# Optimization experiments

Measured on AMD Instinct MI355X. Metric: run time of the kernel, lower is better.

## Reference

```python
import jax, jax.numpy as jnp
import numpy as np

K, STRIDE, PAD, DIL = 3, 1, 1, 1


def setup_inputs() -> dict:
    key = jax.random.key(0)
    k0, k1, k2, k3, k4 = jax.random.split(key, 5)
    B, Cin, Cout, H, W = 16, 64, 64, 64, 64
    x = jax.random.normal(k0, (B, Cin, H, W), dtype=jnp.float32)
    # NOTE: the torch module zero-inits conv_offset; we use small random
    # weights so the deformable sampling path is actually exercised.
    w_off = jax.random.normal(k1, (2 * K * K, Cin, K, K), dtype=jnp.float32) * 0.01
    b_off = jax.random.normal(k2, (2 * K * K,), dtype=jnp.float32) * 0.01
    fan_in = Cin * K * K
    w_dcn = jax.random.normal(k3, (Cout, Cin, K, K), dtype=jnp.float32) / np.sqrt(fan_in)
    b_dcn = jax.random.normal(k4, (Cout,), dtype=jnp.float32) * 0.01
    return {"x": x, "w_off": w_off, "b_off": b_off, "w_dcn": w_dcn, "b_dcn": b_dcn}


def _conv2d(x, w, b, stride, pad):
    out = jax.lax.conv_general_dilated(
        x, w, window_strides=(stride, stride), padding=[(pad, pad), (pad, pad)],
        dimension_numbers=("NCHW", "OIHW", "NCHW"))
    return out + b[None, :, None, None]


def _deform_conv(x, offset, w, b, stride, pad, dil):
    # torchvision-style DeformConv2d, groups=1, no modulation mask.
    B, Cin, H, W = x.shape
    Cout = w.shape[0]
    Ho = (H + 2 * pad - dil * (K - 1) - 1) // stride + 1
    Wo = (W + 2 * pad - dil * (K - 1) - 1) // stride + 1
    KK = K * K
    # base sampling grid: p0 + dilation*kernel_tap + learned offset
    oy = (jnp.arange(Ho) * stride - pad).astype(x.dtype)
    ox = (jnp.arange(Wo) * stride - pad).astype(x.dtype)
    ky, kx = jnp.meshgrid(jnp.arange(K), jnp.arange(K), indexing="ij")
    ky = (ky * dil).reshape(-1).astype(x.dtype)  # [KK], row (y) of tap
    kx = (kx * dil).reshape(-1).astype(x.dtype)
    # offset channel layout: [y_0, x_0, y_1, x_1, ...] -> [B, KK, 2, Ho, Wo]
    off = offset.reshape(B, KK, 2, Ho, Wo)
    py = off[:, :, 0] + ky[None, :, None, None] + oy[None, None, :, None]  # [B,KK,Ho,Wo]
    px = off[:, :, 1] + kx[None, :, None, None] + ox[None, None, None, :]
    y0 = jnp.floor(py)
    x0 = jnp.floor(px)
    wy1 = py - y0
    wx1 = px - x0
    wy0 = 1.0 - wy1
    wx0 = 1.0 - wx1
    x_flat = x.reshape(B, Cin, H * W)

    def gather(yi, xi):
        valid = (yi >= 0) & (yi < H) & (xi >= 0) & (xi < W)  # zero padding outside
        yc = jnp.clip(yi, 0, H - 1).astype(jnp.int32)
        xc = jnp.clip(xi, 0, W - 1).astype(jnp.int32)
        idx = (yc * W + xc).reshape(B, 1, -1)
        v = jnp.take_along_axis(x_flat, idx, axis=2).reshape(B, Cin, KK, Ho, Wo)
        return v * valid.astype(x.dtype).reshape(B, 1, KK, Ho, Wo)

    cols = (gather(y0, x0) * (wy0 * wx0)[:, None]
            + gather(y0, x0 + 1) * (wy0 * wx1)[:, None]
            + gather(y0 + 1, x0) * (wy1 * wx0)[:, None]
            + gather(y0 + 1, x0 + 1) * (wy1 * wx1)[:, None])  # [B,Cin,KK,Ho,Wo]
    out = jnp.einsum("bckhw,ock->bohw", cols, w.reshape(Cout, Cin, KK))
    return out + b[None, :, None, None]


def reference(x, w_off, b_off, w_dcn, b_dcn):
    offset = _conv2d(x, w_off, b_off, STRIDE, PAD)
    return _deform_conv(x, offset, w_dcn, b_dcn, STRIDE, PAD, DIL)
```

## Files before the change

### kernel.cpp

```cpp
#include <hip/hip_runtime.h>
#include <hip/hip_fp16.h>


#define KOFF 18
#define CPAD 72
#define GSTR 33

#define W2T_HALFS    (18 * 64 * 32)
#define WOFF2T_HALFS (18 * 32 * 32)
#define W2T_BYTES    (W2T_HALFS * 2)
#define WOFF2T_OFF   W2T_BYTES
#define X_OFF        (W2T_BYTES + WOFF2T_HALFS * 2)
#define XH_BYTES     (16 * 64 * 64 * 64 * 2)
#define WS_NEED      (X_OFF + XH_BYTES)

typedef _Float16 half8 __attribute__((ext_vector_type(8)));
typedef float floatx4 __attribute__((ext_vector_type(4)));

union H8 { half8 v; __half2 h2[4]; uint4 u; };

__global__ void prep(const float* __restrict__ x,
                     const float* __restrict__ w_dcn,
                     const float* __restrict__ w_off,
                     _Float16* __restrict__ w2t,
                     _Float16* __restrict__ woff2t,
                     _Float16* __restrict__ xh) {
    const int bi = blockIdx.x;
    const int t  = threadIdx.x;
    if (bi < 1024) {
        const int b = bi >> 6, y = bi & 63;
        __shared__ __align__(16) _Float16 tile[64 * CPAD];
        const int xx = t & 63;
        const int c4 = t >> 6;
        const float* xp = x + (((size_t)b * 64) * 64 + y) * 64;
#pragma unroll
        for (int p = 0; p < 16; ++p) {
            int cin = p * 4 + c4;
            tile[xx * CPAD + cin] = (_Float16)xp[(size_t)cin * 4096 + xx];
        }
        __syncthreads();
        const int oct = t & 7;
        const int xl  = t >> 3;
        _Float16* op = xh + ((((size_t)b * 64 + y) * 64) << 6);
#pragma unroll
        for (int p = 0; p < 2; ++p) {
            int xr = p * 32 + xl;
            half8 v = *(const half8*)&tile[xr * CPAD + oct * 8];
            *(half8*)&op[(size_t)xr * 64 + oct * 8] = v;
        }
    } else {
        int e = (bi - 1024) * 256 + t;
        if (e < W2T_HALFS) {
            int kl = e & 31, co = (e >> 5) & 63, i = e >> 11;
            int tap = i >> 1, cin = (i & 1) * 32 + kl;
            w2t[e] = (_Float16)w_dcn[co * 576 + cin * 9 + tap];
        } else {
            int e2 = e - W2T_HALFS;
            int kl = e2 & 31, co = (e2 >> 5) & 31, i = e2 >> 10;
            int tap = i >> 1, cin = (i & 1) * 32 + kl;
            woff2t[e2] = (co < KOFF) ? (_Float16)w_off[co * 576 + cin * 9 + tap]
                                     : (_Float16)0.f;
        }
    }
}

__launch_bounds__(256, 4)
__global__ void dcn_main(const _Float16* __restrict__ xh,
                         const _Float16* __restrict__ w2t,
                         const _Float16* __restrict__ woff2t,
                         const float* __restrict__ b_off,
                         const float* __restrict__ b_dcn,
                         float* __restrict__ out) {
    const int bid = blockIdx.x;
    const int s   = bid >> 3;
    const int b   = ((bid & 7) << 1) | (s >> 7);
    const int ho  = (s >> 1) & 63;
    const int hlf = s & 1;
    const int t    = threadIdx.x;
    const int lane = t & 63;
    const int wid  = __builtin_amdgcn_readfirstlane(t >> 6);
    const int r    = lane & 15;
    const int q    = lane >> 4;
    const int gpx  = t >> 3;
    const int oct  = t & 7;
    const int pxg  = hlf * 32;

    __shared__ __align__(16) _Float16 colsT[2][32 * CPAD];
    __shared__ __align__(16) float    offlds[KOFF * 32];
    __shared__ __align__(16) uint4    grecL[9 * GSTR];

    const _Float16* xb = xh + ((size_t)b << 18);
    const char* xpb = (const char*)xb;

    {
        floatx4 am = {0.f, 0.f, 0.f, 0.f};
        const int m = wid & 1, n = wid >> 1;

        auto loadS = [&](int tap) -> half8 {
            const int dy = tap / 3, dxk = tap - dy * 3;
            const int y  = ho + dy - 1;
            const int xc = pxg + gpx + dxk - 1;
            half8 v = {};
            if (((unsigned)y < 64u) && ((unsigned)xc < 64u))
                v = *(const half8*)&xb[(((size_t)y * 64 + xc) << 6) + oct * 8];
            return v;
        };
        auto loadWA = [&](int tap, int g) -> half8 {
            return *(const half8*)&woff2t[(tap * 2 + g) * 1024
                                          + (m * 16 + r) * 32 + q * 8];
        };

        half8 sv = loadS(0);
        *(half8*)&colsT[0][gpx * CPAD + oct * 8] = sv;
        half8 a0 = loadWA(0, 0), a1 = loadWA(0, 1);
        __syncthreads();
#pragma unroll
        for (int tap = 0; tap < 9; ++tap) {
            half8 sn, a0n, a1n;
            if (tap < 8) {
                sn  = loadS(tap + 1);
                a0n = loadWA(tap + 1, 0);
                a1n = loadWA(tap + 1, 1);
            }
            half8 bf0 = *(const half8*)&colsT[tap & 1][(n * 16 + r) * CPAD + q * 8];
            half8 bf1 = *(const half8*)&colsT[tap & 1][(n * 16 + r) * CPAD + 32 + q * 8];
            am = __builtin_amdgcn_mfma_f32_16x16x32_f16(a0, bf0, am, 0, 0, 0);
            am = __builtin_amdgcn_mfma_f32_16x16x32_f16(a1, bf1, am, 0, 0, 0);
            if (tap < 8) {
                *(half8*)&colsT[(tap + 1) & 1][gpx * CPAD + oct * 8] = sn;
                a0 = a0n; a1 = a1n;
            }
            __syncthreads();
        }
#pragma unroll
        for (int reg = 0; reg < 4; ++reg) {
            int co = m * 16 + q * 4 + reg;
            if (co < KOFF)
                offlds[co * 32 + n * 16 + r] = am[reg] + b_off[co];
        }
    }
    __syncthreads();

    for (int e = t; e < 9 * 32; e += 256) {
        int tap = e >> 5, px = e & 31;
        float offy = offlds[(2 * tap) * 32 + px];
        float offx = offlds[(2 * tap + 1) * 32 + px];
        float py  = offy + (float)(tap / 3) + (float)(ho - 1);
        float pxf = offx + (float)(tap % 3) + (float)(pxg + px - 1);
        float fy = floorf(py), fx = floorf(pxf);
        int y0 = (int)fy, x0 = (int)fx;
        float wy1 = py - fy, wx1 = pxf - fx;
        float wy0 = 1.f - wy1, wx0 = 1.f - wx1;
        bool y0ok = ((unsigned)y0 < 64u);
        bool x0ok = ((unsigned)x0 < 64u);
        bool y1ok = ((unsigned)(y0 + 1) < 64u);
        bool x1ok = ((unsigned)(x0 + 1) < 64u);
        float w00 = (y0ok && x0ok) ? wy0 * wx0 : 0.f;
        float w01 = (y0ok && x1ok) ? wy0 * wx1 : 0.f;
        float w10 = (y1ok && x0ok) ? wy1 * wx0 : 0.f;
        float w11 = (y1ok && x1ok) ? wy1 * wx1 : 0.f;
        int yc0 = min(max(y0, 0), 63);
        int xc0 = min(max(x0, 0), 63);
        int yc1 = min(max(y0 + 1, 0), 63);
        int xc1 = min(max(x0 + 1, 0), 63);
        union { __half2 h; unsigned u; } c0, c1;
        c0.h = __floats2half2_rn(w00, w01);
        c1.h = __floats2half2_rn(w10, w11);
        uint4 rec;
        rec.x = (unsigned)(yc0 * 64 + xc0)
              | ((unsigned)(xc1 - xc0) << 12)
              | ((unsigned)(yc1 - yc0) << 13);
        rec.y = c0.u;
        rec.z = c1.u;
        rec.w = 0u;
        grecL[tap * GSTR + px] = rec;
    }
    __syncthreads();

    floatx4 acc0 = {0.f, 0.f, 0.f, 0.f};
    floatx4 acc1 = {0.f, 0.f, 0.f, 0.f};

    struct G { H8 a, c, d, e; unsigned wy, wz; };

    auto loadB = [&](int tap) -> G {
        uint4 rec = grecL[tap * GSTR + gpx];
        unsigned a00 = (rec.x & 0xfffu) * 128u + (unsigned)oct * 16u;
        unsigned dx128  = ((rec.x >> 12) & 1u) * 128u;
        unsigned dy8192 = ((rec.x >> 13) & 1u) * 8192u;
        G g;
        g.a.v = *(const half8*)(xpb + a00);
        g.c.v = *(const half8*)(xpb + a00 + dx128);
        g.d.v = *(const half8*)(xpb + a00 + dy8192);
        g.e.v = *(const half8*)(xpb + a00 + dy8192 + dx128);
        g.wy = rec.y; g.wz = rec.z;
        return g;
    };
    auto storeB = [&](int tap, G& g) {
        union { unsigned u; __half2 h; } cy, cz;
        cy.u = g.wy; cz.u = g.wz;
        __half2 W00 = __half2half2(__low2half(cy.h));
        __half2 W01 = __half2half2(__high2half(cy.h));
        __half2 W10 = __half2half2(__low2half(cz.h));
        __half2 W11 = __half2half2(__high2half(cz.h));
        H8 res;
#pragma unroll
        for (int c = 0; c < 4; ++c) {
            __half2 aa = __hmul2(g.a.h2[c], W00);
            aa = __hfma2(g.c.h2[c], W01, aa);
            aa = __hfma2(g.d.h2[c], W10, aa);
            aa = __hfma2(g.e.h2[c], W11, aa);
            res.h2[c] = aa;
        }
        *(half8*)&colsT[tap & 1][gpx * CPAD + oct * 8] = res.v;
    };
    auto loadW = [&](int tap, int g) -> half8 {
        return *(const half8*)&w2t[(size_t)(tap * 2 + g) * 2048
                                   + (wid * 16 + r) * 32 + q * 8];
    };

    {
        G g0 = loadB(0);
        storeB(0, g0);
    }
    half8 af0 = loadW(0, 0), af1 = loadW(0, 1);
    __syncthreads();
#pragma unroll
    for (int tap = 0; tap < 9; ++tap) {
        G gn;
        half8 af0n, af1n;
        if (tap < 8) {
            gn   = loadB(tap + 1);
            af0n = loadW(tap + 1, 0);
            af1n = loadW(tap + 1, 1);
        }
        half8 b00 = *(const half8*)&colsT[tap & 1][r * CPAD + q * 8];
        half8 b10 = *(const half8*)&colsT[tap & 1][(16 + r) * CPAD + q * 8];
        half8 b01 = *(const half8*)&colsT[tap & 1][r * CPAD + 32 + q * 8];
        half8 b11 = *(const half8*)&colsT[tap & 1][(16 + r) * CPAD + 32 + q * 8];
        acc0 = __builtin_amdgcn_mfma_f32_16x16x32_f16(af0, b00, acc0, 0, 0, 0);
        acc1 = __builtin_amdgcn_mfma_f32_16x16x32_f16(af0, b10, acc1, 0, 0, 0);
        acc0 = __builtin_amdgcn_mfma_f32_16x16x32_f16(af1, b01, acc0, 0, 0, 0);
        acc1 = __builtin_amdgcn_mfma_f32_16x16x32_f16(af1, b11, acc1, 0, 0, 0);
        if (tap < 8) {
            storeB(tap + 1, gn);
            af0 = af0n; af1 = af1n;
            __syncthreads();
        }
    }

#pragma unroll
    for (int reg = 0; reg < 4; ++reg) {
        int co = wid * 16 + q * 4 + reg;
        float bias = b_dcn[co];
        size_t o = (((size_t)b * 64 + co) * 64 + ho) * 64 + pxg;
        out[o + r]      = acc0[reg] + bias;
        out[o + 16 + r] = acc1[reg] + bias;
    }
}

#define FCPAD 40
__launch_bounds__(256, 4)
__global__ void dcn_fb(const float* __restrict__ x,
                       const float* __restrict__ w_dcn,
                       const float* __restrict__ w_off,
                       const float* __restrict__ b_off,
                       const float* __restrict__ b_dcn,
                       float* __restrict__ out) {
    const int bid = blockIdx.x;
    const int s   = bid >> 3;
    const int b   = ((bid & 7) << 1) | (s >> 7);
    const int ho  = (s >> 1) & 63;
    const int hlf = s & 1;
    const int t    = threadIdx.x;
    const int lane = t & 63;
    const int wid  = __builtin_amdgcn_readfirstlane(t >> 6);
    const int r    = lane & 15;
    const int q    = lane >> 4;
    const int px   = t & 31;
    const int kq   = t >> 5;

    __shared__ __align__(16) _Float16 colsT[2][32 * FCPAD];
    __shared__ __align__(16) float    offlds[KOFF * 32];

    const float* xb = x + (size_t)b * 64 * 4096;
    const int pxg = hlf * 32;

    {
        floatx4 am = {0.f, 0.f, 0.f, 0.f};
        const int m = wid & 1, n = wid >> 1;
        auto stageA = [&](int i) {
            const int tap = i >> 1;
            const int dy = tap / 3, dxk = tap - dy * 3;
            const int y  = ho + dy - 1;
            const int xc = pxg + px + dxk - 1;
            const bool ok = ((unsigned)y < 64u) && ((unsigned)xc < 64u);
            const float* xp = xb + ((size_t)((i & 1) * 32 + kq * 4)) * 4096
                                 + y * 64 + xc;
            float va[4];
#pragma unroll
            for (int j = 0; j < 4; ++j) va[j] = ok ? xp[(size_t)j * 4096] : 0.f;
#pragma unroll
            for (int j = 0; j < 4; ++j)
                colsT[i & 1][px * FCPAD + kq * 4 + j] = (_Float16)va[j];
        };
        auto loadA = [&](int i) -> half8 {
            const int tap = i >> 1;
            const int cin0 = (i & 1) * 32 + q * 8;
            const int co = m * 16 + r;
            half8 v;
#pragma unroll
            for (int j = 0; j < 8; ++j)
                v[j] = (co < KOFF) ? (_Float16)w_off[co * 576 + (cin0 + j) * 9 + tap]
                                   : (_Float16)0.f;
            return v;
        };
        stageA(0);
        __syncthreads();
#pragma unroll
        for (int i = 0; i < 18; ++i) {
            if (i < 17) stageA(i + 1);
            half8 a = loadA(i);
            half8 bfr = *(const half8*)&colsT[i & 1][(n * 16 + r) * FCPAD + q * 8];
            am = __builtin_amdgcn_mfma_f32_16x16x32_f16(a, bfr, am, 0, 0, 0);
            __syncthreads();
        }
#pragma unroll
        for (int reg = 0; reg < 4; ++reg) {
            int co = m * 16 + q * 4 + reg;
            if (co < KOFF)
                offlds[co * 32 + (n * 16 + r)] = am[reg] + b_off[co];
        }
    }
    __syncthreads();

    unsigned rmeta[9], rw0[9], rw1[9];
#pragma unroll
    for (int tap = 0; tap < 9; ++tap) {
        float offy = offlds[(2 * tap) * 32 + px];
        float offx = offlds[(2 * tap + 1) * 32 + px];
        float py  = offy + (float)(tap / 3) + (float)(ho - 1);
        float pxf = offx + (float)(tap % 3) + (float)(pxg + px - 1);
        float fy = floorf(py), fx = floorf(pxf);
        int y0 = (int)fy, x0 = (int)fx;
        float wy1 = py - fy, wx1 = pxf - fx;
        float wy0 = 1.f - wy1, wx0 = 1.f - wx1;
        bool y0ok = ((unsigned)y0 < 64u);
        bool x0ok = ((unsigned)x0 < 64u);
        bool y1ok = ((unsigned)(y0 + 1) < 64u);
        bool x1ok = ((unsigned)(x0 + 1) < 64u);
        float w00 = (y0ok && x0ok) ? wy0 * wx0 : 0.f;
        float w01 = (y0ok && x1ok) ? wy0 * wx1 : 0.f;
        float w10 = (y1ok && x0ok) ? wy1 * wx0 : 0.f;
        float w11 = (y1ok && x1ok) ? wy1 * wx1 : 0.f;
        int yc0 = min(max(y0, 0), 63);
        int xc0 = min(max(x0, 0), 63);
        int yc1 = min(max(y0 + 1, 0), 63);
        int xc1 = min(max(x0 + 1, 0), 63);
        union { __half2 h; unsigned u; } c0, c1;
        c0.h = __floats2half2_rn(w00, w01);
        c1.h = __floats2half2_rn(w10, w11);
        rmeta[tap] = (unsigned)(yc0 * 64 + xc0)
                   | ((unsigned)(xc1 - xc0) << 12)
                   | ((unsigned)(yc1 - yc0) << 13);
        rw0[tap] = c0.u;
        rw1[tap] = c1.u;
    }

    floatx4 acc0 = {0.f, 0.f, 0.f, 0.f};
    floatx4 acc1 = {0.f, 0.f, 0.f, 0.f};

    auto gather = [&](int i) {
        const int tap = i >> 1;
        const unsigned m = rmeta[tap];
        const unsigned a00 = (m & 0xfffu) << 2;
        const unsigned a01 = a00 + ((m >> 10) & 4u);
        const unsigned a10 = a00 + ((m >> 5) & 256u);
        const unsigned a11 = a10 + ((m >> 10) & 4u);
        const char* base = (const char*)xb
                         + ((size_t)((i & 1) * 32 + kq * 4)) * 16384;
        float v00[4], v01[4], v10[4], v11[4];
#pragma unroll
        for (int j = 0; j < 4; ++j) {
            const char* xp = base + (size_t)j * 16384;
            v00[j] = *(const float*)(xp + a00);
            v01[j] = *(const float*)(xp + a01);
            v10[j] = *(const float*)(xp + a10);
            v11[j] = *(const float*)(xp + a11);
        }
        union { unsigned u; __half2 h; } c0, c1;
        c0.u = rw0[tap]; c1.u = rw1[tap];
        const float wA = __half2float(c0.h.x), wB = __half2float(c0.h.y);
        const float wC = __half2float(c1.h.x), wD = __half2float(c1.h.y);
#pragma unroll
        for (int j = 0; j < 4; ++j)
            colsT[i & 1][px * FCPAD + kq * 4 + j] =
                (_Float16)(v00[j] * wA + v01[j] * wB + v10[j] * wC + v11[j] * wD);
    };

    auto load_af = [&](int i) -> half8 {
        const int tap = i >> 1;
        const int cin0 = (i & 1) * 32 + q * 8;
        half8 v;
#pragma unroll
        for (int j = 0; j < 8; ++j)
            v[j] = (_Float16)w_dcn[(wid * 16 + r) * 576 + (cin0 + j) * 9 + tap];
        return v;
    };

    gather(0);
    __syncthreads();
#pragma unroll
    for (int i = 0; i < 18; ++i) {
        if (i < 17) gather(i + 1);
        half8 af = load_af(i);
        half8 b0 = *(const half8*)&colsT[i & 1][r * FCPAD + q * 8];
        half8 b1 = *(const half8*)&colsT[i & 1][(16 + r) * FCPAD + q * 8];
        acc0 = __builtin_amdgcn_mfma_f32_16x16x32_f16(af, b0, acc0, 0, 0, 0);
        acc1 = __builtin_amdgcn_mfma_f32_16x16x32_f16(af, b1, acc1, 0, 0, 0);
        if (i < 17) __syncthreads();
    }

#pragma unroll
    for (int reg = 0; reg < 4; ++reg) {
        int co = wid * 16 + q * 4 + reg;
        float bias = b_dcn[co];
        size_t o = (((size_t)b * 64 + co) * 64 + ho) * 64 + pxg;
        out[o + r]      = acc0[reg] + bias;
        out[o + 16 + r] = acc1[reg] + bias;
    }
}

extern "C" void kernel_launch(void* const* d_in, const int* in_sizes, int n_in,
                              void* d_out, int out_size, void* d_ws, size_t ws_size,
                              hipStream_t stream) {
    const float* x     = (const float*)d_in[0];
    const float* w_off = (const float*)d_in[1];
    const float* b_off = (const float*)d_in[2];
    const float* w_dcn = (const float*)d_in[3];
    const float* b_dcn = (const float*)d_in[4];
    float* out = (float*)d_out;

    char* ws = (char*)d_ws;
    _Float16* w2t    = (_Float16*)ws;
    _Float16* woff2t = (_Float16*)(ws + WOFF2T_OFF);
    _Float16* xh     = (_Float16*)(ws + X_OFF);

    if (ws_size >= (size_t)WS_NEED) {
        prep<<<1240, 256, 0, stream>>>(x, w_dcn, w_off, w2t, woff2t, xh);
        dcn_main<<<2048, 256, 0, stream>>>(xh, w2t, woff2t, b_off, b_dcn, out);
    } else {
        dcn_fb<<<2048, 256, 0, stream>>>(x, w_dcn, w_off, b_off, b_dcn, out);
    }
}
```

Baseline: 110.2 us.

## Process two taps per pipeline stage to halve barriers in offset and deform GEMMs

Both the offset-conv and deformable-conv MFMA loops now stage two kernel taps per double-buffered LDS slot, with the column tile widened to 128 halfs plus padding. This cuts the number of __syncthreads from nine to five per phase and gives more independent gathers and MFMAs between barriers, so load latency can be hidden better. In exchange it doubles the bilinear gather registers in flight and grows LDS usage, which may lower occupancy.

```diff
diff --git a/kernel.cpp b/kernel.cpp
--- a/kernel.cpp
+++ b/kernel.cpp
@@ -3,7 +3,7 @@
 
 
 #define KOFF 18
-#define CPAD 72
+#define CTS  136
 #define GSTR 33
 
 #define W2T_HALFS    (18 * 64 * 32)
@@ -29,14 +29,14 @@
     const int t  = threadIdx.x;
     if (bi < 1024) {
         const int b = bi >> 6, y = bi & 63;
-        __shared__ __align__(16) _Float16 tile[64 * CPAD];
+        __shared__ __align__(16) _Float16 tile[64 * 72];
         const int xx = t & 63;
         const int c4 = t >> 6;
         const float* xp = x + (((size_t)b * 64) * 64 + y) * 64;
 #pragma unroll
         for (int p = 0; p < 16; ++p) {
             int cin = p * 4 + c4;
-            tile[xx * CPAD + cin] = (_Float16)xp[(size_t)cin * 4096 + xx];
+            tile[xx * 72 + cin] = (_Float16)xp[(size_t)cin * 4096 + xx];
         }
         __syncthreads();
         const int oct = t & 7;
@@ -45,7 +45,7 @@
 #pragma unroll
         for (int p = 0; p < 2; ++p) {
             int xr = p * 32 + xl;
-            half8 v = *(const half8*)&tile[xr * CPAD + oct * 8];
+            half8 v = *(const half8*)&tile[xr * 72 + oct * 8];
             *(half8*)&op[(size_t)xr * 64 + oct * 8] = v;
         }
     } else {
@@ -85,7 +85,7 @@
     const int oct  = t & 7;
     const int pxg  = hlf * 32;
 
-    __shared__ __align__(16) _Float16 colsT[2][32 * CPAD];
+    __shared__ __align__(16) _Float16 colsT[2][32 * CTS];
     __shared__ __align__(16) float    offlds[KOFF * 32];
     __shared__ __align__(16) uint4    grecL[9 * GSTR];
 
@@ -105,32 +105,39 @@
                 v = *(const half8*)&xb[(((size_t)y * 64 + xc) << 6) + oct * 8];
             return v;
         };
-        auto loadWA = [&](int tap, int g) -> half8 {
-            return *(const half8*)&woff2t[(tap * 2 + g) * 1024
-                                          + (m * 16 + r) * 32 + q * 8];
+        auto loadWA = [&](int i) -> half8 {
+            return *(const half8*)&woff2t[i * 1024 + (m * 16 + r) * 32 + q * 8];
         };
 
-        half8 sv = loadS(0);
-        *(half8*)&colsT[0][gpx * CPAD + oct * 8] = sv;
-        half8 a0 = loadWA(0, 0), a1 = loadWA(0, 1);
+        {
+            half8 s0 = loadS(0), s1 = loadS(1);
+            *(half8*)&colsT[0][gpx * CTS + oct * 8]      = s0;
+            *(half8*)&colsT[0][gpx * CTS + 64 + oct * 8] = s1;
+        }
         __syncthreads();
 #pragma unroll
-        for (int tap = 0; tap < 9; ++tap) {
-            half8 sn, a0n, a1n;
-            if (tap < 8) {
-                sn  = loadS(tap + 1);
-                a0n = loadWA(tap + 1, 0);
-                a1n = loadWA(tap + 1, 1);
-            }
-            half8 bf0 = *(const half8*)&colsT[tap & 1][(n * 16 + r) * CPAD + q * 8];
-            half8 bf1 = *(const half8*)&colsT[tap & 1][(n * 16 + r) * CPAD + 32 + q * 8];
-            am = __builtin_amdgcn_mfma_f32_16x16x32_f16(a0, bf0, am, 0, 0, 0);
-            am = __builtin_amdgcn_mfma_f32_16x16x32_f16(a1, bf1, am, 0, 0, 0);
-            if (tap < 8) {
-                *(half8*)&colsT[(tap + 1) & 1][gpx * CPAD + oct * 8] = sn;
-                a0 = a0n; a1 = a1n;
-            }
-            __syncthreads();
+        for (int p = 0; p < 5; ++p) {
+            half8 sn0, sn1;
+            if (p < 4) {
+                sn0 = loadS(2 * p + 2);
+                if (p < 3) sn1 = loadS(2 * p + 3);
+            }
+            const int nkg = (p < 4) ? 4 : 2;
+#pragma unroll
+            for (int kg = 0; kg < 4; ++kg) {
+                if (kg < nkg) {
+                    half8 a  = loadWA(4 * p + kg);
+                    half8 bf = *(const half8*)&colsT[p & 1][(n * 16 + r) * CTS
+                                                            + kg * 32 + q * 8];
+                    am = __builtin_amdgcn_mfma_f32_16x16x32_f16(a, bf, am, 0, 0, 0);
+                }
+            }
+            if (p < 4) {
+                *(half8*)&colsT[(p + 1) & 1][gpx * CTS + oct * 8] = sn0;
+                if (p < 3)
+                    *(half8*)&colsT[(p + 1) & 1][gpx * CTS + 64 + oct * 8] = sn1;
+                __syncthreads();
+            }
         }
 #pragma unroll
         for (int reg = 0; reg < 4; ++reg) {
@@ -180,70 +187,90 @@
     floatx4 acc0 = {0.f, 0.f, 0.f, 0.f};
     floatx4 acc1 = {0.f, 0.f, 0.f, 0.f};
 
-    struct G { H8 a, c, d, e; unsigned wy, wz; };
-
-    auto loadB = [&](int tap) -> G {
-        uint4 rec = grecL[tap * GSTR + gpx];
-        unsigned a00 = (rec.x & 0xfffu) * 128u + (unsigned)oct * 16u;
-        unsigned dx128  = ((rec.x >> 12) & 1u) * 128u;
-        unsigned dy8192 = ((rec.x >> 13) & 1u) * 8192u;
-        G g;
-        g.a.v = *(const half8*)(xpb + a00);
-        g.c.v = *(const half8*)(xpb + a00 + dx128);
-        g.d.v = *(const half8*)(xpb + a00 + dy8192);
-        g.e.v = *(const half8*)(xpb + a00 + dy8192 + dx128);
-        g.wy = rec.y; g.wz = rec.z;
+    struct GP { H8 v[8]; unsigned wy0, wz0, wy1, wz1; };
+
+    auto loadPairB = [&](int p) -> GP {
+        GP g;
+#pragma unroll
+        for (int l = 0; l < 2; ++l) {
+            int tap = 2 * p + l;
+            if (tap < 9) {
+                uint4 rec = grecL[tap * GSTR + gpx];
+                unsigned a00 = (rec.x & 0xfffu) * 128u + (unsigned)oct * 16u;
+                unsigned dx128  = ((rec.x >> 12) & 1u) * 128u;
+                unsigned dy8192 = ((rec.x >> 13) & 1u) * 8192u;
+                g.v[4 * l + 0].v = *(const half8*)(xpb + a00);
+                g.v[4 * l + 1].v = *(const half8*)(xpb + a00 + dx128);
+                g.v[4 * l + 2].v = *(const half8*)(xpb + a00 + dy8192);
+                g.v[4 * l + 3].v = *(const half8*)(xpb + a00 + dy8192 + dx128);
+                if (l == 0) { g.wy0 = rec.y; g.wz0 = rec.z; }
+                else        { g.wy1 = rec.y; g.wz1 = rec.z; }
+            }
+        }
         return g;
     };
-    auto storeB = [&](int tap, G& g) {
-        union { unsigned u; __half2 h; } cy, cz;
-        cy.u = g.wy; cz.u = g.wz;
-        __half2 W00 = __half2half2(__low2half(cy.h));
-        __half2 W01 = __half2half2(__high2half(cy.h));
-        __half2 W10 = __half2half2(__low2half(cz.h));
-        __half2 W11 = __half2half2(__high2half(cz.h));
-        H8 res;
-#pragma unroll
-        for (int c = 0; c < 4; ++c) {
-            __half2 aa = __hmul2(g.a.h2[c], W00);
-            aa = __hfma2(g.c.h2[c], W01, aa);
-            aa = __hfma2(g.d.h2[c], W10, aa);
-            aa = __hfma2(g.e.h2[c], W11, aa);
-            res.h2[c] = aa;
-        }
-        *(half8*)&colsT[tap & 1][gpx * CPAD + oct * 8] = res.v;
+    auto storePairB = [&](int p, int buf, GP& g) {
+#pragma unroll
+        for (int l = 0; l < 2; ++l) {
+            int tap = 2 * p + l;
+            if (tap < 9) {
+                union { unsigned u; __half2 h; } cy, cz;
+                cy.u = l ? g.wy1 : g.wy0;
+                cz.u = l ? g.wz1 : g.wz0;
+                __half2 W00 = __half2half2(__low2half(cy.h));
+                __half2 W01 = __half2half2(__high2half(cy.h));
+                __half2 W10 = __half2half2(__low2half(cz.h));
+                __half2 W11 = __half2half2(__high2half(cz.h));
+                H8 res;
+#pragma unroll
+                for (int c = 0; c < 4; ++c) {
+                    __half2 aa = __hmul2(g.v[4 * l + 0].h2[c], W00);
+                    aa = __hfma2(g.v[4 * l + 1].h2[c], W01, aa);
+                    aa = __hfma2(g.v[4 * l + 2].h2[c], W10, aa);
+                    aa = __hfma2(g.v[4 * l + 3].h2[c], W11, aa);
+                    res.h2[c] = aa;
+                }
+                *(half8*)&colsT[buf][gpx * CTS + l * 64 + oct * 8] = res.v;
+            }
+        }
     };
-    auto loadW = [&](int tap, int g) -> half8 {
-        return *(const half8*)&w2t[(size_t)(tap * 2 + g) * 2048
-                                   + (wid * 16 + r) * 32 + q * 8];
+    auto loadW = [&](int i) -> half8 {
+        return *(const half8*)&w2t[(size_t)i * 2048 + (wid * 16 + r) * 32 + q * 8];
     };
 
     {
-        G g0 = loadB(0);
-        storeB(0, g0);
-    }
-    half8 af0 = loadW(0, 0), af1 = loadW(0, 1);
+        GP g0 = loadPairB(0);
+        storePairB(0, 0, g0);
+    }
+    half8 wf[4];
+#pragma unroll
+    for (int kg = 0; kg < 4; ++kg) wf[kg] = loadW(kg);
     __syncthreads();
-#pragma unroll
-    for (int tap = 0; tap < 9; ++tap) {
-        G gn;
-        half8 af0n, af1n;
-        if (tap < 8) {
-            gn   = loadB(tap + 1);
-            af0n = loadW(tap + 1, 0);
-            af1n = loadW(tap + 1, 1);
-        }
-        half8 b00 = *(const half8*)&colsT[tap & 1][r * CPAD + q * 8];
-        half8 b10 = *(const half8*)&colsT[tap & 1][(16 + r) * CPAD + q * 8];
-        half8 b01 = *(const half8*)&colsT[tap & 1][r * CPAD + 32 + q * 8];
-        half8 b11 = *(const half8*)&colsT[tap & 1][(16 + r) * CPAD + 32 + q * 8];
-        acc0 = __builtin_amdgcn_mfma_f32_16x16x32_f16(af0, b00, acc0, 0, 0, 0);
-        acc1 = __builtin_amdgcn_mfma_f32_16x16x32_f16(af0, b10, acc1, 0, 0, 0);
-        acc0 = __builtin_amdgcn_mfma_f32_16x16x32_f16(af1, b01, acc0, 0, 0, 0);
-        acc1 = __builtin_amdgcn_mfma_f32_16x16x32_f16(af1, b11, acc1, 0, 0, 0);
-        if (tap < 8) {
-            storeB(tap + 1, gn);
-            af0 = af0n; af1 = af1n;
+
+#pragma unroll
+    for (int p = 0; p < 5; ++p) {
+        GP gn;
+        half8 wfn[4];
+        if (p < 4) {
+            gn = loadPairB(p + 1);
+#pragma unroll
+            for (int kg = 0; kg < 4; ++kg)
+                if (4 * (p + 1) + kg < 18) wfn[kg] = loadW(4 * (p + 1) + kg);
+        }
+        const int nkg = (p < 4) ? 4 : 2;
+#pragma unroll
+        for (int kg = 0; kg < 4; ++kg) {
+            if (kg < nkg) {
+                half8 b0 = *(const half8*)&colsT[p & 1][r * CTS + kg * 32 + q * 8];
+                half8 b1 = *(const half8*)&colsT[p & 1][(16 + r) * CTS + kg * 32 + q * 8];
+                acc0 = __builtin_amdgcn_mfma_f32_16x16x32_f16(wf[kg], b0, acc0, 0, 0, 0);
+                acc1 = __builtin_amdgcn_mfma_f32_16x16x32_f16(wf[kg], b1, acc1, 0, 0, 0);
+            }
+        }
+        if (p < 4) {
+            storePairB(p + 1, (p + 1) & 1, gn);
+#pragma unroll
+            for (int kg = 0; kg < 4; ++kg) wf[kg] = wfn[kg];
             __syncthreads();
         }
     }
```

Measured after the change: 108.4 us (median of 2 runs). No clear change (-1.6%).
